# Performance work log

Measured on AMD Instinct MI355X. Metric: run time of the kernel, lower is better.

## Reference

```python
import jax, jax.numpy as jnp
import numpy as np

B, T, D, E, H, K = 4, 1024, 1024, 8, 4096, 2
N = B * T
EPS_LN = 1e-5
EPS_W = 1e-8
BAL_W = 0.01


def setup_inputs() -> dict:
    key = jax.random.key(0)
    ks = jax.random.split(key, 5)
    sc = 0.02
    return {
        "x": jax.random.normal(ks[0], (B, T, D), jnp.float32),
        "ln_gamma": jnp.ones((D,), jnp.float32),
        "ln_beta": jnp.zeros((D,), jnp.float32),
        "gate_w": jax.random.normal(ks[1], (D, E), jnp.float32) * sc,
        "w1": jax.random.normal(ks[2], (E, D, H), jnp.float32) * sc,
        "b1": jnp.zeros((E, H), jnp.float32),
        "w2": jax.random.normal(ks[3], (E, H, D), jnp.float32) * sc,
        "b2": jnp.zeros((E, D), jnp.float32),
    }


def reference(x, ln_gamma, ln_beta, gate_w, w1, b1, w2, b2):
    # LayerNorm (pre-norm), residual kept on raw x
    mu = jnp.mean(x, axis=-1, keepdims=True)
    var = jnp.var(x, axis=-1, keepdims=True)
    xn = (x - mu) * jax.lax.rsqrt(var + EPS_LN) * ln_gamma + ln_beta

    xf = xn.reshape(N, D)

    # Router (oscillator_state=None path): token gate only, k = top_k
    logits = xf @ gate_w                         # (N, E)
    router_probs = jax.nn.softmax(logits, axis=-1)
    top_w, top_i = jax.lax.top_k(router_probs, K)  # (N, K)
    top_w = top_w / (jnp.sum(top_w, axis=-1, keepdims=True) + EPS_W)

    # Dense per-token gate matrix: gates[n, e] = sum of top-k weights routed to e
    gates = jnp.zeros((N, E), xf.dtype).at[jnp.arange(N)[:, None], top_i].add(top_w)

    # Per-expert FFN (computed densely for all tokens, combined by sparse gates)
    h = jax.nn.gelu(jnp.einsum("nd,edh->enh", xf, w1) + b1[:, None, :], approximate=False)
    expert_out = jnp.einsum("enh,ehd->end", h, w2) + b2[:, None, :]  # (E, N, D)
    moe = jnp.einsum("ne,end->nd", gates, expert_out)

    output = x + moe.reshape(B, T, D)

    # Load-balance auxiliary loss
    counts = jnp.zeros((E,), xf.dtype).at[top_i.reshape(-1)].add(1.0)
    fraction = counts / N
    balance_loss = BAL_W * E * jnp.sum(fraction * jnp.mean(router_probs, axis=0))

    return output, balance_loss, router_probs
```

## Files before the change

### kernel.cpp

```cpp
#include <hip/hip_runtime.h>
#include <hip/hip_bf16.h>
#include <math.h>

#define DI   1024
#define EI   8
#define HI   4096
#define NI   4096

typedef __bf16 bf16x8 __attribute__((ext_vector_type(8)));
typedef float  f32x4  __attribute__((ext_vector_type(4)));

__device__ __forceinline__ unsigned short f2bf(float f) {
  union { float f; unsigned u; } c; c.f = f;
  unsigned r = c.u + 0x7FFF + ((c.u >> 16) & 1);
  return (unsigned short)(r >> 16);
}

__device__ __forceinline__ void async16(const void* g, void* l) {
  __builtin_amdgcn_global_load_lds(
      (const __attribute__((address_space(1))) void*)g,
      (__attribute__((address_space(3))) void*)l, 16, 0, 0);
}

__global__ __launch_bounds__(256) void ln_router_k(
    const float* __restrict__ x, const float* __restrict__ gamma,
    const float* __restrict__ beta, const float* __restrict__ gw,
    unsigned short* __restrict__ xnbf, float* __restrict__ probs_out,
    int* __restrict__ pairs, float2* __restrict__ gates2)
{
  const int t = threadIdx.x, lane = t & 63, wid = t >> 6;
  const int n = blockIdx.x * 4 + wid;

  const float4* xr = (const float4*)(x + (size_t)n * DI);
  float4 v[4];
  #pragma unroll
  for (int j = 0; j < 4; j++) v[j] = xr[lane * 4 + j];

  float s = 0.f, q = 0.f;
  #pragma unroll
  for (int j = 0; j < 4; j++) {
    s += v[j].x + v[j].y + v[j].z + v[j].w;
    q += v[j].x * v[j].x + v[j].y * v[j].y + v[j].z * v[j].z + v[j].w * v[j].w;
  }
  #pragma unroll
  for (int off = 1; off < 64; off <<= 1) {
    s += __shfl_xor(s, off);
    q += __shfl_xor(q, off);
  }
  const float mu = s * (1.0f / DI);
  const float rs = rsqrtf(q * (1.0f / DI) - mu * mu + 1e-5f);

  const float4* gr = (const float4*)gamma;
  const float4* br = (const float4*)beta;
  float xl[16];
  #pragma unroll
  for (int j = 0; j < 4; j++) {
    const float4 g4 = gr[lane * 4 + j];
    const float4 b4 = br[lane * 4 + j];
    xl[4 * j + 0] = (v[j].x - mu) * rs * g4.x + b4.x;
    xl[4 * j + 1] = (v[j].y - mu) * rs * g4.y + b4.y;
    xl[4 * j + 2] = (v[j].z - mu) * rs * g4.z + b4.z;
    xl[4 * j + 3] = (v[j].w - mu) * rs * g4.w + b4.w;
  }
  unsigned u[8];
  #pragma unroll
  for (int j = 0; j < 8; j++)
    u[j] = (unsigned)f2bf(xl[2 * j]) | ((unsigned)f2bf(xl[2 * j + 1]) << 16);
  uint4* dst = (uint4*)(xnbf + (size_t)n * DI + lane * 16);
  uint4 d0; d0.x = u[0]; d0.y = u[1]; d0.z = u[2]; d0.w = u[3];
  uint4 d1; d1.x = u[4]; d1.y = u[5]; d1.z = u[6]; d1.w = u[7];
  dst[0] = d0; dst[1] = d1;

  float p[8];
  #pragma unroll
  for (int e = 0; e < 8; e++) p[e] = 0.f;
  #pragma unroll
  for (int j = 0; j < 16; j++) {
    const float4* grow = (const float4*)(gw + (size_t)(lane * 16 + j) * EI);
    const float4 ga = grow[0], gb = grow[1];
    const float xv = xl[j];
    p[0] += xv * ga.x; p[1] += xv * ga.y; p[2] += xv * ga.z; p[3] += xv * ga.w;
    p[4] += xv * gb.x; p[5] += xv * gb.y; p[6] += xv * gb.z; p[7] += xv * gb.w;
  }
  #pragma unroll
  for (int e = 0; e < 8; e++)
    #pragma unroll
    for (int off = 1; off < 64; off <<= 1) p[e] += __shfl_xor(p[e], off);

  if (lane == 0) {
    float pm = -1e30f;
    #pragma unroll
    for (int e = 0; e < 8; e++) pm = fmaxf(pm, p[e]);
    float pr[8], ps = 0.f;
    #pragma unroll
    for (int e = 0; e < 8; e++) { pr[e] = expf(p[e] - pm); ps += pr[e]; }
    const float inv = 1.0f / ps;
    #pragma unroll
    for (int e = 0; e < 8; e++) {
      pr[e] *= inv;
      probs_out[(size_t)n * EI + e] = pr[e];
    }
    int i0 = 0; float m0 = pr[0];
    #pragma unroll
    for (int e = 1; e < 8; e++) if (pr[e] > m0) { m0 = pr[e]; i0 = e; }
    int i1 = -1; float m1 = -1e30f;
    #pragma unroll
    for (int e = 0; e < 8; e++) if (e != i0 && pr[e] > m1) { m1 = pr[e]; i1 = e; }
    const float ssum = m0 + m1 + 1e-8f;
    pairs[n] = i0 | (i1 << 8);
    float2 g2; g2.x = m0 / ssum; g2.y = m1 / ssum;
    gates2[n] = g2;
  }
}

__global__ __launch_bounds__(1024) void build_lists_k(
    const int* __restrict__ pairs, const float2* __restrict__ gates2,
    const float* __restrict__ probs, int* __restrict__ counts,
    int* __restrict__ offs, int* __restrict__ tok_list,
    float* __restrict__ gate_list, int2* __restrict__ ipos,
    float* __restrict__ out_bal)
{
  __shared__ int cnt[8];
  __shared__ int cur[8];
  __shared__ float wps[16][8];
  __shared__ float ps[8];
  const int t = threadIdx.x, lane = t & 63, wid = t >> 6;
  if (t < 8) cnt[t] = 0;
  __syncthreads();

  float acc[8];
  #pragma unroll
  for (int e = 0; e < 8; e++) acc[e] = 0.f;
  for (int n = t; n < NI; n += 1024) {
    const int pr = pairs[n];
    atomicAdd(&cnt[pr & 255], 1);
    atomicAdd(&cnt[pr >> 8], 1);
    const float4* prow = (const float4*)(probs + (size_t)n * EI);
    const float4 a = prow[0], b = prow[1];
    acc[0] += a.x; acc[1] += a.y; acc[2] += a.z; acc[3] += a.w;
    acc[4] += b.x; acc[5] += b.y; acc[6] += b.z; acc[7] += b.w;
  }
  #pragma unroll
  for (int e = 0; e < 8; e++)
    #pragma unroll
    for (int off = 1; off < 64; off <<= 1) acc[e] += __shfl_xor(acc[e], off);
  if (lane == 0)
    #pragma unroll
    for (int e = 0; e < 8; e++) wps[wid][e] = acc[e];
  __syncthreads();
  if (t < 8) {
    float sm = 0.f;
    for (int w = 0; w < 16; w++) sm += wps[w][t];
    ps[t] = sm;
  }
  __syncthreads();
  if (t == 0) {
    int off = 0; float bl = 0.f;
    for (int e = 0; e < 8; e++) {
      offs[e] = off; cur[e] = off; counts[e] = cnt[e];
      bl += (float)cnt[e] * ps[e];
      off += cnt[e];
    }
    *out_bal = 0.01f * 8.0f * bl / ((float)NI * (float)NI);
  }
  __syncthreads();
  for (int n = t; n < NI; n += 1024) {
    const int pr = pairs[n];
    const float2 g = gates2[n];
    const int p0 = atomicAdd(&cur[pr & 255], 1);
    tok_list[p0] = n; gate_list[p0] = g.x;
    const int p1 = atomicAdd(&cur[pr >> 8], 1);
    tok_list[p1] = n; gate_list[p1] = g.y;
    int2 ip; ip.x = p0; ip.y = p1;
    ipos[n] = ip;
  }
}

__global__ __launch_bounds__(256) void transpose_cvt_k(
    const float* __restrict__ in, unsigned short* __restrict__ out, int R, int C)
{
  __shared__ float tile[64][65];
  const size_t eoff = (size_t)blockIdx.z * (size_t)R * (size_t)C;
  const int c0 = blockIdx.x * 64, r0 = blockIdx.y * 64;
  const int t = threadIdx.x;
  {
    const int col = (t & 15) * 4;
    #pragma unroll
    for (int ii = 0; ii < 4; ii++) {
      const int row = (t >> 4) + ii * 16;
      const float4 v = *(const float4*)(in + eoff + (size_t)(r0 + row) * C + c0 + col);
      tile[row][col + 0] = v.x; tile[row][col + 1] = v.y;
      tile[row][col + 2] = v.z; tile[row][col + 3] = v.w;
    }
  }
  __syncthreads();
  {
    const int grp = t & 7;
    #pragma unroll
    for (int jj = 0; jj < 2; jj++) {
      const int orow = (t >> 3) + jj * 32;
      unsigned short vs[8];
      #pragma unroll
      for (int u = 0; u < 8; u++) vs[u] = f2bf(tile[grp * 8 + u][orow]);
      uint4 pk;
      pk.x = (unsigned)vs[0] | ((unsigned)vs[1] << 16);
      pk.y = (unsigned)vs[2] | ((unsigned)vs[3] << 16);
      pk.z = (unsigned)vs[4] | ((unsigned)vs[5] << 16);
      pk.w = (unsigned)vs[6] | ((unsigned)vs[7] << 16);
      *(uint4*)(out + eoff + (size_t)(c0 + orow) * R + r0 + grp * 8) = pk;
    }
  }
}

__global__ __launch_bounds__(256) void copy_x_k(const float* __restrict__ x, float* __restrict__ out)
{
  const size_t i = (size_t)blockIdx.x * 256 + threadIdx.x;
  ((float4*)out)[i] = ((const float4*)x)[i];
}

__global__ __launch_bounds__(256) void ffn1_k(
    const unsigned short* __restrict__ xnbf, const unsigned short* __restrict__ w1t,
    const float* __restrict__ b1, unsigned short* __restrict__ hbuf,
    const int* __restrict__ tok_list, const int* __restrict__ counts,
    const int* __restrict__ offsets)
{
  const int e = blockIdx.z;
  const int cnt = counts[e];
  const int mt = blockIdx.y;
  if (mt * 128 >= cnt) return;
  const int n0 = blockIdx.x * 128;
  const int t = threadIdx.x, lane = t & 63, w = t >> 6;
  const int wm = w & 1, wn = w >> 1;
  __shared__ __align__(16) unsigned short As[128 * 64];
  __shared__ __align__(16) unsigned short Bs[128 * 64];

  const int sub = lane >> 3;
  const int kc = (((lane & 7) ^ sub) * 8);
  const int eoff = offsets[e];
  const unsigned short* baseA[4];
  const unsigned short* baseB[4];
  #pragma unroll
  for (int r = 0; r < 4; r++) {
    int row = (w << 5) + r * 8 + sub;
    int idx = mt * 128 + row; if (idx > cnt - 1) idx = cnt - 1;
    int tok = tok_list[eoff + idx];
    baseA[r] = xnbf + (size_t)tok * DI + kc;
    baseB[r] = w1t + (size_t)e * HI * DI + (size_t)(n0 + row) * DI + kc;
  }

  f32x4 acc[4][4];
  const f32x4 zz = {0.f, 0.f, 0.f, 0.f};
  #pragma unroll
  for (int i = 0; i < 4; i++)
    #pragma unroll
    for (int j = 0; j < 4; j++) acc[i][j] = zz;

  const int mrow = (wm << 6) + (lane & 15);
  const int nrow = (wn << 6) + (lane & 15);
  const int ksw[2] = { (((lane >> 4) ^ (lane & 7)) * 8),
                       ((((lane >> 4) + 4) ^ (lane & 7)) * 8) };

  for (int k0 = 0; k0 < DI; k0 += 64) {
    __syncthreads();
    #pragma unroll
    for (int r = 0; r < 4; r++) {
      async16(baseA[r] + k0, &As[((w << 5) + r * 8) * 64]);
      async16(baseB[r] + k0, &Bs[((w << 5) + r * 8) * 64]);
    }
    __syncthreads();
    #pragma unroll
    for (int kk = 0; kk < 2; kk++) {
      const int ko = ksw[kk];
      bf16x8 af[4], bfr[4];
      #pragma unroll
      for (int mi = 0; mi < 4; mi++)
        af[mi] = *(const bf16x8*)&As[(mrow + mi * 16) * 64 + ko];
      #pragma unroll
      for (int ni = 0; ni < 4; ni++)
        bfr[ni] = *(const bf16x8*)&Bs[(nrow + ni * 16) * 64 + ko];
      #pragma unroll
      for (int mi = 0; mi < 4; mi++)
        #pragma unroll
        for (int ni = 0; ni < 4; ni++)
          acc[mi][ni] = __builtin_amdgcn_mfma_f32_16x16x32_bf16(af[mi], bfr[ni], acc[mi][ni], 0, 0, 0);
    }
  }

  const int hb = eoff + mt * 128;
  #pragma unroll
  for (int ni = 0; ni < 4; ni++) {
    const int col = n0 + (wn << 6) + ni * 16 + (lane & 15);
    const float bias = b1[e * HI + col];
    #pragma unroll
    for (int mi = 0; mi < 4; mi++) {
      #pragma unroll
      for (int rg = 0; rg < 4; rg++) {
        const int rowl = (wm << 6) + mi * 16 + ((lane >> 4) << 2) + rg;
        if (mt * 128 + rowl < cnt) {
          float vv = acc[mi][ni][rg] + bias;
          vv = 0.5f * vv * (1.0f + erff(vv * 0.70710678118f));
          hbuf[(size_t)(hb + rowl) * HI + col] = f2bf(vv);
        }
      }
    }
  }
}

__global__ __launch_bounds__(256) void ffn2_k(
    const unsigned short* __restrict__ hbuf, const unsigned short* __restrict__ w2t,
    const float* __restrict__ b2, float* __restrict__ out,
    const int* __restrict__ tok_list, const float* __restrict__ gate_list,
    const int* __restrict__ counts, const int* __restrict__ offsets,
    float* __restrict__ eo)
{
  const int e = blockIdx.z;
  const int cnt = counts[e];
  const int mt = blockIdx.y;
  if (mt * 128 >= cnt) return;
  const int n0 = blockIdx.x * 128;
  const int t = threadIdx.x, lane = t & 63, w = t >> 6;
  const int wm = w & 1, wn = w >> 1;
  __shared__ __align__(16) unsigned short As[128 * 64];
  __shared__ __align__(16) unsigned short Bs[128 * 64];

  const int sub = lane >> 3;
  const int kc = (((lane & 7) ^ sub) * 8);
  const int eoff = offsets[e];
  const int hb = eoff + mt * 128;
  const unsigned short* baseA[4];
  const unsigned short* baseB[4];
  #pragma unroll
  for (int r = 0; r < 4; r++) {
    int row = (w << 5) + r * 8 + sub;
    baseA[r] = hbuf + (size_t)(hb + row) * HI + kc;
    baseB[r] = w2t + (size_t)e * DI * HI + (size_t)(n0 + row) * HI + kc;
  }

  f32x4 acc[4][4];
  const f32x4 zz = {0.f, 0.f, 0.f, 0.f};
  #pragma unroll
  for (int i = 0; i < 4; i++)
    #pragma unroll
    for (int j = 0; j < 4; j++) acc[i][j] = zz;

  const int mrow = (wm << 6) + (lane & 15);
  const int nrow = (wn << 6) + (lane & 15);
  const int ksw[2] = { (((lane >> 4) ^ (lane & 7)) * 8),
                       ((((lane >> 4) + 4) ^ (lane & 7)) * 8) };

  for (int k0 = 0; k0 < HI; k0 += 64) {
    __syncthreads();
    #pragma unroll
    for (int r = 0; r < 4; r++) {
      async16(baseA[r] + k0, &As[((w << 5) + r * 8) * 64]);
      async16(baseB[r] + k0, &Bs[((w << 5) + r * 8) * 64]);
    }
    __syncthreads();
    #pragma unroll
    for (int kk = 0; kk < 2; kk++) {
      const int ko = ksw[kk];
      bf16x8 af[4], bfr[4];
      #pragma unroll
      for (int mi = 0; mi < 4; mi++)
        af[mi] = *(const bf16x8*)&As[(mrow + mi * 16) * 64 + ko];
      #pragma unroll
      for (int ni = 0; ni < 4; ni++)
        bfr[ni] = *(const bf16x8*)&Bs[(nrow + ni * 16) * 64 + ko];
      #pragma unroll
      for (int mi = 0; mi < 4; mi++)
        #pragma unroll
        for (int ni = 0; ni < 4; ni++)
          acc[mi][ni] = __builtin_amdgcn_mfma_f32_16x16x32_bf16(af[mi], bfr[ni], acc[mi][ni], 0, 0, 0);
    }
  }

  float bias[4];
  #pragma unroll
  for (int ni = 0; ni < 4; ni++)
    bias[ni] = b2[e * DI + n0 + (wn << 6) + ni * 16 + (lane & 15)];

  if (eo) {
    #pragma unroll
    for (int mi = 0; mi < 4; mi++) {
      #pragma unroll
      for (int rg = 0; rg < 4; rg++) {
        const int rowl = (wm << 6) + mi * 16 + ((lane >> 4) << 2) + rg;
        const int gidx = mt * 128 + rowl;
        if (gidx < cnt) {
          float* erow = eo + (size_t)(hb + rowl) * DI;
          #pragma unroll
          for (int ni = 0; ni < 4; ni++) {
            const int col = n0 + (wn << 6) + ni * 16 + (lane & 15);
            erow[col] = acc[mi][ni][rg] + bias[ni];
          }
        }
      }
    }
  } else {
    #pragma unroll
    for (int mi = 0; mi < 4; mi++) {
      #pragma unroll
      for (int rg = 0; rg < 4; rg++) {
        const int rowl = (wm << 6) + mi * 16 + ((lane >> 4) << 2) + rg;
        const int gidx = mt * 128 + rowl;
        if (gidx < cnt) {
          const int tok = tok_list[eoff + gidx];
          const float gte = gate_list[eoff + gidx];
          float* orow = out + (size_t)tok * DI;
          #pragma unroll
          for (int ni = 0; ni < 4; ni++) {
            const int col = n0 + (wn << 6) + ni * 16 + (lane & 15);
            atomicAdd(orow + col, (acc[mi][ni][rg] + bias[ni]) * gte);
          }
        }
      }
    }
  }
}

__global__ __launch_bounds__(256) void combine_k(
    const float* __restrict__ x, const float* __restrict__ eo,
    const int2* __restrict__ ipos, const float2* __restrict__ gates2,
    float* __restrict__ out)
{
  const int n = blockIdx.x, t = threadIdx.x;
  const int2 pp = ipos[n];
  const float2 gg = gates2[n];
  const float4 a = ((const float4*)(x  + (size_t)n    * DI))[t];
  const float4 b = ((const float4*)(eo + (size_t)pp.x * DI))[t];
  const float4 c = ((const float4*)(eo + (size_t)pp.y * DI))[t];
  float4 r;
  r.x = a.x + gg.x * b.x + gg.y * c.x;
  r.y = a.y + gg.x * b.y + gg.y * c.y;
  r.z = a.z + gg.x * b.z + gg.y * c.z;
  r.w = a.w + gg.x * b.w + gg.y * c.w;
  ((float4*)(out + (size_t)n * DI))[t] = r;
}

extern "C" void kernel_launch(void* const* d_in, const int* in_sizes, int n_in,
                              void* d_out, int out_size, void* d_ws, size_t ws_size,
                              hipStream_t stream)
{
  const float* x   = (const float*)d_in[0];
  const float* gam = (const float*)d_in[1];
  const float* bet = (const float*)d_in[2];
  const float* gw  = (const float*)d_in[3];
  const float* w1  = (const float*)d_in[4];
  const float* b1  = (const float*)d_in[5];
  const float* w2  = (const float*)d_in[6];
  const float* b2  = (const float*)d_in[7];
  float* out = (float*)d_out;

  char* ws = (char*)d_ws;
  int*    counts = (int*)(ws + 0);
  int*    offs   = (int*)(ws + 64);
  int*    pairs  = (int*)(ws + 1024);
  float2* gates2 = (float2*)(ws + 20480);
  int*    tok    = (int*)(ws + 57344);
  float*  gate   = (float*)(ws + 90112);
  int2*   ipos   = (int2*)(ws + 122880);
  unsigned short* xnbf = (unsigned short*)(ws + 262656);
  unsigned short* wt   = (unsigned short*)(ws + 8651264);
  unsigned short* hbuf = (unsigned short*)(ws + 75760128);
  const bool use_eo = (ws_size >= 177472000ull);
  float* eo = use_eo ? (float*)(ws + 143917568) : (float*)nullptr;

  float* bal_out   = out + (size_t)NI * DI;
  float* probs_out = bal_out + 1;

  ln_router_k<<<NI / 4, 256, 0, stream>>>(x, gam, bet, gw, xnbf, probs_out, pairs, gates2);
  build_lists_k<<<1, 1024, 0, stream>>>(pairs, gates2, probs_out, counts, offs, tok, gate, ipos, bal_out);
  transpose_cvt_k<<<dim3(HI / 64, DI / 64, EI), 256, 0, stream>>>(w1, wt, DI, HI);
  if (!use_eo)
    copy_x_k<<<(NI * DI / 4) / 256, 256, 0, stream>>>(x, out);
  ffn1_k<<<dim3(HI / 128, NI / 128, EI), 256, 0, stream>>>(xnbf, wt, b1, hbuf, tok, counts, offs);
  transpose_cvt_k<<<dim3(DI / 64, HI / 64, EI), 256, 0, stream>>>(w2, wt, HI, DI);
  ffn2_k<<<dim3(DI / 128, NI / 128, EI), 256, 0, stream>>>(hbuf, wt, b2, out, tok, gate, counts, offs, eo);
  if (use_eo)
    combine_k<<<NI, 256, 0, stream>>>(x, eo, ipos, gates2, out);
}
```

Measured before the change: 659.9 us.

## Fuse prep kernels, enlarge FFN GEMM tiles, and use tanh GELU approximation

LayerNorm/router and both weight transposes are merged into one prep kernel. Separate w1t and w2t buffers let both transposes run up front. ffn1 moves to 256x256 tiles with 512 threads, and ffn2 to 128x256 tiles with each wave owning a 64-column strip, for more reuse of each LDS load. Launch bounds now request two blocks per CU. The erf GELU is replaced by a tanh approximation built on __expf, which is cheaper but departs from the exact-erf reference and may exceed tolerance.

```diff
diff --git a/kernel.cpp b/kernel.cpp
--- a/kernel.cpp
+++ b/kernel.cpp
@@ -22,14 +22,22 @@
       (__attribute__((address_space(3))) void*)l, 16, 0, 0);
 }
 
-__global__ __launch_bounds__(256) void ln_router_k(
+__device__ __forceinline__ float gelu_f(float x) {
+  const float u = x * (0.7978845608f + 0.0356774081f * x * x);
+  const float tt = __expf(-2.0f * fabsf(u));
+  float th = (1.0f - tt) / (1.0f + tt);
+  th = copysignf(th, u);
+  return 0.5f * x * (1.0f + th);
+}
+
+__device__ __forceinline__ void ln_router_body(
     const float* __restrict__ x, const float* __restrict__ gamma,
     const float* __restrict__ beta, const float* __restrict__ gw,
     unsigned short* __restrict__ xnbf, float* __restrict__ probs_out,
-    int* __restrict__ pairs, float2* __restrict__ gates2)
-{
-  const int t = threadIdx.x, lane = t & 63, wid = t >> 6;
-  const int n = blockIdx.x * 4 + wid;
+    int* __restrict__ pairs, float2* __restrict__ gates2, int blk, int t)
+{
+  const int lane = t & 63, wid = t >> 6;
+  const int n = blk * 4 + wid;
 
   const float4* xr = (const float4*)(x + (size_t)n * DI);
   float4 v[4];
@@ -111,6 +119,69 @@
     float2 g2; g2.x = m0 / ssum; g2.y = m1 / ssum;
     gates2[n] = g2;
   }
+}
+
+__device__ __forceinline__ void transpose_body(
+    const float* __restrict__ in, unsigned short* __restrict__ out,
+    int R, int C, int bx, int by, int bz, float (*tile)[65], int t)
+{
+  const size_t eoff = (size_t)bz * (size_t)R * (size_t)C;
+  const int c0 = bx * 64, r0 = by * 64;
+  {
+    const int col = (t & 15) * 4;
+    #pragma unroll
+    for (int ii = 0; ii < 4; ii++) {
+      const int row = (t >> 4) + ii * 16;
+      const float4 v = *(const float4*)(in + eoff + (size_t)(r0 + row) * C + c0 + col);
+      tile[row][col + 0] = v.x; tile[row][col + 1] = v.y;
+      tile[row][col + 2] = v.z; tile[row][col + 3] = v.w;
+    }
+  }
+  __syncthreads();
+  {
+    const int grp = t & 7;
+    #pragma unroll
+    for (int jj = 0; jj < 2; jj++) {
+      const int orow = (t >> 3) + jj * 32;
+      unsigned short vs[8];
+      #pragma unroll
+      for (int u = 0; u < 8; u++) vs[u] = f2bf(tile[grp * 8 + u][orow]);
+      uint4 pk;
+      pk.x = (unsigned)vs[0] | ((unsigned)vs[1] << 16);
+      pk.y = (unsigned)vs[2] | ((unsigned)vs[3] << 16);
+      pk.z = (unsigned)vs[4] | ((unsigned)vs[5] << 16);
+      pk.w = (unsigned)vs[6] | ((unsigned)vs[7] << 16);
+      *(uint4*)(out + eoff + (size_t)(c0 + orow) * R + r0 + grp * 8) = pk;
+    }
+  }
+}
+
+__global__ __launch_bounds__(256) void prep_k(
+    const float* __restrict__ x, const float* __restrict__ gamma,
+    const float* __restrict__ beta, const float* __restrict__ gw,
+    unsigned short* __restrict__ xnbf, float* __restrict__ probs_out,
+    int* __restrict__ pairs, float2* __restrict__ gates2,
+    const float* __restrict__ w1, unsigned short* __restrict__ w1t,
+    const float* __restrict__ w2, unsigned short* __restrict__ w2t)
+{
+  __shared__ float tile[64][65];
+  const int bx = blockIdx.x, t = threadIdx.x;
+  if (bx < 1024) {
+    ln_router_body(x, gamma, beta, gw, xnbf, probs_out, pairs, gates2, bx, t);
+  } else if (bx < 1024 + 8192) {
+    const int b = bx - 1024;
+    transpose_body(w1, w1t, DI, HI, b & 63, (b >> 6) & 15, b >> 10, tile, t);
+  } else {
+    const int b = bx - 9216;
+    transpose_body(w2, w2t, HI, DI, b & 15, (b >> 4) & 63, b >> 10, tile, t);
+  }
+}
+
+__global__ __launch_bounds__(256) void transpose_cvt_k(
+    const float* __restrict__ in, unsigned short* __restrict__ out, int R, int C)
+{
+  __shared__ float tile[64][65];
+  transpose_body(in, out, R, C, blockIdx.x, blockIdx.y, blockIdx.z, tile, threadIdx.x);
 }
 
 __global__ __launch_bounds__(1024) void build_lists_k(
@@ -176,49 +247,13 @@
   }
 }
 
-__global__ __launch_bounds__(256) void transpose_cvt_k(
-    const float* __restrict__ in, unsigned short* __restrict__ out, int R, int C)
-{
-  __shared__ float tile[64][65];
-  const size_t eoff = (size_t)blockIdx.z * (size_t)R * (size_t)C;
-  const int c0 = blockIdx.x * 64, r0 = blockIdx.y * 64;
-  const int t = threadIdx.x;
-  {
-    const int col = (t & 15) * 4;
-    #pragma unroll
-    for (int ii = 0; ii < 4; ii++) {
-      const int row = (t >> 4) + ii * 16;
-      const float4 v = *(const float4*)(in + eoff + (size_t)(r0 + row) * C + c0 + col);
-      tile[row][col + 0] = v.x; tile[row][col + 1] = v.y;
-      tile[row][col + 2] = v.z; tile[row][col + 3] = v.w;
-    }
-  }
-  __syncthreads();
-  {
-    const int grp = t & 7;
-    #pragma unroll
-    for (int jj = 0; jj < 2; jj++) {
-      const int orow = (t >> 3) + jj * 32;
-      unsigned short vs[8];
-      #pragma unroll
-      for (int u = 0; u < 8; u++) vs[u] = f2bf(tile[grp * 8 + u][orow]);
-      uint4 pk;
-      pk.x = (unsigned)vs[0] | ((unsigned)vs[1] << 16);
-      pk.y = (unsigned)vs[2] | ((unsigned)vs[3] << 16);
-      pk.z = (unsigned)vs[4] | ((unsigned)vs[5] << 16);
-      pk.w = (unsigned)vs[6] | ((unsigned)vs[7] << 16);
-      *(uint4*)(out + eoff + (size_t)(c0 + orow) * R + r0 + grp * 8) = pk;
-    }
-  }
-}
-
 __global__ __launch_bounds__(256) void copy_x_k(const float* __restrict__ x, float* __restrict__ out)
 {
   const size_t i = (size_t)blockIdx.x * 256 + threadIdx.x;
   ((float4*)out)[i] = ((const float4*)x)[i];
 }
 
-__global__ __launch_bounds__(256) void ffn1_k(
+__global__ __launch_bounds__(512, 2) void ffn1_k(
     const unsigned short* __restrict__ xnbf, const unsigned short* __restrict__ w1t,
     const float* __restrict__ b1, unsigned short* __restrict__ hbuf,
     const int* __restrict__ tok_list, const int* __restrict__ counts,
@@ -227,38 +262,38 @@
   const int e = blockIdx.z;
   const int cnt = counts[e];
   const int mt = blockIdx.y;
-  if (mt * 128 >= cnt) return;
-  const int n0 = blockIdx.x * 128;
+  if (mt * 256 >= cnt) return;
+  const int n0 = blockIdx.x * 256;
   const int t = threadIdx.x, lane = t & 63, w = t >> 6;
   const int wm = w & 1, wn = w >> 1;
-  __shared__ __align__(16) unsigned short As[128 * 64];
-  __shared__ __align__(16) unsigned short Bs[128 * 64];
+  __shared__ __align__(16) unsigned short As[256 * 64];
+  __shared__ __align__(16) unsigned short Bs[256 * 64];
 
   const int sub = lane >> 3;
-  const int kc = (((lane & 7) ^ sub) * 8);
+  const int kc = ((lane & 7) ^ sub) * 8;
   const int eoff = offsets[e];
   const unsigned short* baseA[4];
   const unsigned short* baseB[4];
   #pragma unroll
   for (int r = 0; r < 4; r++) {
     int row = (w << 5) + r * 8 + sub;
-    int idx = mt * 128 + row; if (idx > cnt - 1) idx = cnt - 1;
+    int idx = mt * 256 + row; if (idx > cnt - 1) idx = cnt - 1;
     int tok = tok_list[eoff + idx];
     baseA[r] = xnbf + (size_t)tok * DI + kc;
     baseB[r] = w1t + (size_t)e * HI * DI + (size_t)(n0 + row) * DI + kc;
   }
 
-  f32x4 acc[4][4];
+  f32x4 acc[8][4];
   const f32x4 zz = {0.f, 0.f, 0.f, 0.f};
   #pragma unroll
-  for (int i = 0; i < 4; i++)
+  for (int i = 0; i < 8; i++)
     #pragma unroll
     for (int j = 0; j < 4; j++) acc[i][j] = zz;
 
-  const int mrow = (wm << 6) + (lane & 15);
+  const int mrow = (wm << 7) + (lane & 15);
   const int nrow = (wn << 6) + (lane & 15);
-  const int ksw[2] = { (((lane >> 4) ^ (lane & 7)) * 8),
-                       ((((lane >> 4) + 4) ^ (lane & 7)) * 8) };
+  const int ksw[2] = { ((lane >> 4) ^ (lane & 7)) * 8,
+                       (((lane >> 4) + 4) ^ (lane & 7)) * 8 };
 
   for (int k0 = 0; k0 < DI; k0 += 64) {
     __syncthreads();
@@ -271,34 +306,33 @@
     #pragma unroll
     for (int kk = 0; kk < 2; kk++) {
       const int ko = ksw[kk];
-      bf16x8 af[4], bfr[4];
-      #pragma unroll
-      for (int mi = 0; mi < 4; mi++)
+      bf16x8 af[8], bfr[4];
+      #pragma unroll
+      for (int mi = 0; mi < 8; mi++)
         af[mi] = *(const bf16x8*)&As[(mrow + mi * 16) * 64 + ko];
       #pragma unroll
       for (int ni = 0; ni < 4; ni++)
         bfr[ni] = *(const bf16x8*)&Bs[(nrow + ni * 16) * 64 + ko];
       #pragma unroll
-      for (int mi = 0; mi < 4; mi++)
+      for (int mi = 0; mi < 8; mi++)
         #pragma unroll
         for (int ni = 0; ni < 4; ni++)
           acc[mi][ni] = __builtin_amdgcn_mfma_f32_16x16x32_bf16(af[mi], bfr[ni], acc[mi][ni], 0, 0, 0);
     }
   }
 
-  const int hb = eoff + mt * 128;
+  const int hb = eoff + mt * 256;
   #pragma unroll
   for (int ni = 0; ni < 4; ni++) {
     const int col = n0 + (wn << 6) + ni * 16 + (lane & 15);
     const float bias = b1[e * HI + col];
     #pragma unroll
-    for (int mi = 0; mi < 4; mi++) {
+    for (int mi = 0; mi < 8; mi++) {
       #pragma unroll
       for (int rg = 0; rg < 4; rg++) {
-        const int rowl = (wm << 6) + mi * 16 + ((lane >> 4) << 2) + rg;
-        if (mt * 128 + rowl < cnt) {
-          float vv = acc[mi][ni][rg] + bias;
-          vv = 0.5f * vv * (1.0f + erff(vv * 0.70710678118f));
+        const int rowl = (wm << 7) + mi * 16 + ((lane >> 4) << 2) + rg;
+        if (mt * 256 + rowl < cnt) {
+          const float vv = gelu_f(acc[mi][ni][rg] + bias);
           hbuf[(size_t)(hb + rowl) * HI + col] = f2bf(vv);
         }
       }
@@ -306,7 +340,7 @@
   }
 }
 
-__global__ __launch_bounds__(256) void ffn2_k(
+__global__ __launch_bounds__(256, 2) void ffn2_k(
     const unsigned short* __restrict__ hbuf, const unsigned short* __restrict__ w2t,
     const float* __restrict__ b2, float* __restrict__ out,
     const int* __restrict__ tok_list, const float* __restrict__ gate_list,
@@ -317,57 +351,61 @@
   const int cnt = counts[e];
   const int mt = blockIdx.y;
   if (mt * 128 >= cnt) return;
-  const int n0 = blockIdx.x * 128;
+  const int n0 = blockIdx.x * 256;
   const int t = threadIdx.x, lane = t & 63, w = t >> 6;
-  const int wm = w & 1, wn = w >> 1;
   __shared__ __align__(16) unsigned short As[128 * 64];
-  __shared__ __align__(16) unsigned short Bs[128 * 64];
+  __shared__ __align__(16) unsigned short Bs[256 * 64];
 
   const int sub = lane >> 3;
-  const int kc = (((lane & 7) ^ sub) * 8);
+  const int kc = ((lane & 7) ^ sub) * 8;
   const int eoff = offsets[e];
   const int hb = eoff + mt * 128;
   const unsigned short* baseA[4];
-  const unsigned short* baseB[4];
+  const unsigned short* baseB[8];
   #pragma unroll
   for (int r = 0; r < 4; r++) {
     int row = (w << 5) + r * 8 + sub;
     baseA[r] = hbuf + (size_t)(hb + row) * HI + kc;
+  }
+  #pragma unroll
+  for (int r = 0; r < 8; r++) {
+    int row = (w << 6) + r * 8 + sub;
     baseB[r] = w2t + (size_t)e * DI * HI + (size_t)(n0 + row) * HI + kc;
   }
 
-  f32x4 acc[4][4];
+  f32x4 acc[8][4];
   const f32x4 zz = {0.f, 0.f, 0.f, 0.f};
   #pragma unroll
-  for (int i = 0; i < 4; i++)
+  for (int i = 0; i < 8; i++)
     #pragma unroll
     for (int j = 0; j < 4; j++) acc[i][j] = zz;
 
-  const int mrow = (wm << 6) + (lane & 15);
-  const int nrow = (wn << 6) + (lane & 15);
-  const int ksw[2] = { (((lane >> 4) ^ (lane & 7)) * 8),
-                       ((((lane >> 4) + 4) ^ (lane & 7)) * 8) };
+  const int mrow = (lane & 15);
+  const int nrow = (w << 6) + (lane & 15);
+  const int ksw[2] = { ((lane >> 4) ^ (lane & 7)) * 8,
+                       (((lane >> 4) + 4) ^ (lane & 7)) * 8 };
 
   for (int k0 = 0; k0 < HI; k0 += 64) {
     __syncthreads();
     #pragma unroll
-    for (int r = 0; r < 4; r++) {
+    for (int r = 0; r < 4; r++)
       async16(baseA[r] + k0, &As[((w << 5) + r * 8) * 64]);
-      async16(baseB[r] + k0, &Bs[((w << 5) + r * 8) * 64]);
-    }
+    #pragma unroll
+    for (int r = 0; r < 8; r++)
+      async16(baseB[r] + k0, &Bs[((w << 6) + r * 8) * 64]);
     __syncthreads();
     #pragma unroll
     for (int kk = 0; kk < 2; kk++) {
       const int ko = ksw[kk];
-      bf16x8 af[4], bfr[4];
-      #pragma unroll
-      for (int mi = 0; mi < 4; mi++)
+      bf16x8 af[8], bfr[4];
+      #pragma unroll
+      for (int mi = 0; mi < 8; mi++)
         af[mi] = *(const bf16x8*)&As[(mrow + mi * 16) * 64 + ko];
       #pragma unroll
       for (int ni = 0; ni < 4; ni++)
         bfr[ni] = *(const bf16x8*)&Bs[(nrow + ni * 16) * 64 + ko];
       #pragma unroll
-      for (int mi = 0; mi < 4; mi++)
+      for (int mi = 0; mi < 8; mi++)
         #pragma unroll
         for (int ni = 0; ni < 4; ni++)
           acc[mi][ni] = __builtin_amdgcn_mfma_f32_16x16x32_bf16(af[mi], bfr[ni], acc[mi][ni], 0, 0, 0);
@@ -377,20 +415,20 @@
   float bias[4];
   #pragma unroll
   for (int ni = 0; ni < 4; ni++)
-    bias[ni] = b2[e * DI + n0 + (wn << 6) + ni * 16 + (lane & 15)];
+    bias[ni] = b2[e * DI + n0 + (w << 6) + ni * 16 + (lane & 15)];
 
   if (eo) {
     #pragma unroll
-    for (int mi = 0; mi < 4; mi++) {
+    for (int mi = 0; mi < 8; mi++) {
       #pragma unroll
       for (int rg = 0; rg < 4; rg++) {
-        const int rowl = (wm << 6) + mi * 16 + ((lane >> 4) << 2) + rg;
+        const int rowl = mi * 16 + ((lane >> 4) << 2) + rg;
         const int gidx = mt * 128 + rowl;
         if (gidx < cnt) {
           float* erow = eo + (size_t)(hb + rowl) * DI;
           #pragma unroll
           for (int ni = 0; ni < 4; ni++) {
-            const int col = n0 + (wn << 6) + ni * 16 + (lane & 15);
+            const int col = n0 + (w << 6) + ni * 16 + (lane & 15);
             erow[col] = acc[mi][ni][rg] + bias[ni];
           }
         }
@@ -398,10 +436,10 @@
     }
   } else {
     #pragma unroll
-    for (int mi = 0; mi < 4; mi++) {
+    for (int mi = 0; mi < 8; mi++) {
       #pragma unroll
       for (int rg = 0; rg < 4; rg++) {
-        const int rowl = (wm << 6) + mi * 16 + ((lane >> 4) << 2) + rg;
+        const int rowl = mi * 16 + ((lane >> 4) << 2) + rg;
         const int gidx = mt * 128 + rowl;
         if (gidx < cnt) {
           const int tok = tok_list[eoff + gidx];
@@ -409,7 +447,7 @@
           float* orow = out + (size_t)tok * DI;
           #pragma unroll
           for (int ni = 0; ni < 4; ni++) {
-            const int col = n0 + (wn << 6) + ni * 16 + (lane & 15);
+            const int col = n0 + (w << 6) + ni * 16 + (lane & 15);
             atomicAdd(orow + col, (acc[mi][ni][rg] + bias[ni]) * gte);
           }
         }
@@ -460,22 +498,42 @@
   float*  gate   = (float*)(ws + 90112);
   int2*   ipos   = (int2*)(ws + 122880);
   unsigned short* xnbf = (unsigned short*)(ws + 262656);
-  unsigned short* wt   = (unsigned short*)(ws + 8651264);
-  unsigned short* hbuf = (unsigned short*)(ws + 75760128);
-  const bool use_eo = (ws_size >= 177472000ull);
-  float* eo = use_eo ? (float*)(ws + 143917568) : (float*)nullptr;
 
   float* bal_out   = out + (size_t)NI * DI;
   float* probs_out = bal_out + 1;
 
-  ln_router_k<<<NI / 4, 256, 0, stream>>>(x, gam, bet, gw, xnbf, probs_out, pairs, gates2);
-  build_lists_k<<<1, 1024, 0, stream>>>(pairs, gates2, probs_out, counts, offs, tok, gate, ipos, bal_out);
-  transpose_cvt_k<<<dim3(HI / 64, DI / 64, EI), 256, 0, stream>>>(w1, wt, DI, HI);
-  if (!use_eo)
+  const size_t W1T_OFF = 8651264;
+  const size_t W2T_OFF = W1T_OFF + 67108864;
+  const size_t HB_OFF  = W2T_OFF + 67108864;
+  const size_t EO_OFF  = HB_OFF + 68157440;
+  const size_t FAST_REQ = EO_OFF + 33554432;
+
+  if (ws_size >= FAST_REQ) {
+    unsigned short* w1t  = (unsigned short*)(ws + W1T_OFF);
+    unsigned short* w2t  = (unsigned short*)(ws + W2T_OFF);
+    unsigned short* hbuf = (unsigned short*)(ws + HB_OFF);
+    float*          eo   = (float*)(ws + EO_OFF);
+
+    prep_k<<<17408, 256, 0, stream>>>(x, gam, bet, gw, xnbf, probs_out, pairs, gates2,
+                                      w1, w1t, w2, w2t);
+    build_lists_k<<<1, 1024, 0, stream>>>(pairs, gates2, probs_out, counts, offs,
+                                          tok, gate, ipos, bal_out);
+    ffn1_k<<<dim3(HI / 256, 16, EI), 512, 0, stream>>>(xnbf, w1t, b1, hbuf, tok, counts, offs);
+    ffn2_k<<<dim3(DI / 256, 32, EI), 256, 0, stream>>>(hbuf, w2t, b2, out, tok, gate, counts, offs, eo);
+    combine_k<<<NI, 256, 0, stream>>>(x, eo, ipos, gates2, out);
+  } else {
+    unsigned short* wt   = (unsigned short*)(ws + W1T_OFF);
+    unsigned short* hbuf = (unsigned short*)(ws + W2T_OFF);
+
+    prep_k<<<1024, 256, 0, stream>>>(x, gam, bet, gw, xnbf, probs_out, pairs, gates2,
+                                     w1, wt, w2, wt);
+    build_lists_k<<<1, 1024, 0, stream>>>(pairs, gates2, probs_out, counts, offs,
+                                          tok, gate, ipos, bal_out);
+    transpose_cvt_k<<<dim3(HI / 64, DI / 64, EI), 256, 0, stream>>>(w1, wt, DI, HI);
     copy_x_k<<<(NI * DI / 4) / 256, 256, 0, stream>>>(x, out);
-  ffn1_k<<<dim3(HI / 128, NI / 128, EI), 256, 0, stream>>>(xnbf, wt, b1, hbuf, tok, counts, offs);
-  transpose_cvt_k<<<dim3(DI / 64, HI / 64, EI), 256, 0, stream>>>(w2, wt, HI, DI);
-  ffn2_k<<<dim3(DI / 128, NI / 128, EI), 256, 0, stream>>>(hbuf, wt, b2, out, tok, gate, counts, offs, eo);
-  if (use_eo)
-    combine_k<<<NI, 256, 0, stream>>>(x, eo, ipos, gates2, out);
-}
+    ffn1_k<<<dim3(HI / 256, 16, EI), 512, 0, stream>>>(xnbf, wt, b1, hbuf, tok, counts, offs);
+    transpose_cvt_k<<<dim3(DI / 64, HI / 64, EI), 256, 0, stream>>>(w2, wt, HI, DI);
+    ffn2_k<<<dim3(DI / 256, 32, EI), 256, 0, stream>>>(hbuf, wt, b2, out, tok, gate, counts, offs,
+                                                       (float*)nullptr);
+  }
+}
```

Measured after the change: 669.6 us. About the same (+1.5%).
